# Kernel tuning notes

Measured on AMD Instinct MI355X. Metric: run time of the kernel, lower is better.

Reference implementation:

```python
import jax, jax.numpy as jnp
import numpy as np

H, I, E, TOPK = 2048, 4096, 8, 2
B, S = 2, 2048

def setup_inputs() -> dict:
    key = jax.random.key(0)
    ks = jax.random.split(key, 6)
    x = jax.random.normal(ks[0], (B, S, H), dtype=jnp.float32)
    expert_indices = jax.random.randint(ks[1], (B, S, TOPK), 0, E, dtype=jnp.int64)
    expert_weights = jax.random.uniform(ks[2], (B, S, TOPK), dtype=jnp.float32)
    gate_proj = jax.random.normal(ks[3], (E, I, H), dtype=jnp.float32) * 0.02
    up_proj = jax.random.normal(ks[4], (E, I, H), dtype=jnp.float32) * 0.02
    down_proj = jax.random.normal(ks[5], (E, H, I), dtype=jnp.float32) * 0.02
    return {"x": x, "expert_indices": expert_indices, "expert_weights": expert_weights,
            "gate_proj": gate_proj, "up_proj": up_proj, "down_proj": down_proj}

def reference(x, expert_indices, expert_weights, gate_proj, up_proj, down_proj):
    b, s, h = x.shape
    T = b * s
    xf = x.reshape(T, h)                                   # [T, H]
    idx = expert_indices.reshape(T, -1)                    # [T, K]
    w = expert_weights.reshape(T, -1)                      # [T, K]
    n_exp = gate_proj.shape[0]
    # Per-token combined weight for each expert (sums duplicate slots, matching
    # the original weighted scatter-add over (token, slot) pairs).
    onehot = jax.nn.one_hot(idx, n_exp, dtype=xf.dtype)    # [T, K, E]
    we = jnp.einsum('tk,tke->et', w, onehot)               # [E, T]

    def step(acc, inp):
        g_w, u_w, d_w, w_e = inp                           # [I,H], [I,H], [H,I], [T]
        g = xf @ g_w.T                                     # [T, I]
        u = xf @ u_w.T                                     # [T, I]
        inter = g * jax.nn.sigmoid(g) * u                  # fused SiLU(g) * u
        acc = acc + w_e[:, None] * (inter @ d_w.T)         # weighted combine
        return acc, None

    out0 = jnp.zeros((T, h), dtype=x.dtype)
    out, _ = jax.lax.scan(step, out0, (gate_proj, up_proj, down_proj, we))
    return out.reshape(b, s, h)
```

## Files before the change

### kernel.cpp

```cpp
#include <hip/hip_runtime.h>
#include <hip/hip_bf16.h>
#include <stdint.h>

#define H_DIM 2048
#define I_DIM 4096
#define NEXP  8
#define NTOK  4096
#define NPAIR 8192
#define PAD_ROWS (NPAIR + 256)

#define MiB (1024ull * 1024ull)
#define WS_COUNTS   0ull
#define WS_OFFSETS  256ull
#define WS_TOKID    1024ull
#define WS_SLOT     (64ull * 1024)
#define WS_PAIRW    (128ull * 1024)
#define WS_XG       (1ull * MiB)
#define WS_INTER    (36ull * MiB)
#define WS_Y        (104ull * MiB)
#define WS_GW       (176ull * MiB)
#define WS_UW       (304ull * MiB)
#define WS_DW       (432ull * MiB)
#define WS_FULL     (560ull * MiB)

typedef __attribute__((ext_vector_type(8))) short bf16x8;
typedef __attribute__((ext_vector_type(4))) float f32x4;

#if defined(__has_builtin)
#if __has_builtin(__builtin_amdgcn_cvt_pk_bf16_f32)
#define HAVE_CVT_PK 1
#endif
#endif

__device__ __forceinline__ uint32_t bf16_bits_rne(float x) {
  uint32_t u = __float_as_uint(x);
  return (u + 0x7FFFu + ((u >> 16) & 1u)) >> 16;
}
__device__ __forceinline__ uint32_t pk_bf16(float a, float b) {
#ifdef HAVE_CVT_PK
  auto r = __builtin_amdgcn_cvt_pk_bf16_f32(a, b);
  return __builtin_bit_cast(uint32_t, r);
#else
  return bf16_bits_rne(a) | (bf16_bits_rne(b) << 16);
#endif
}
__device__ __forceinline__ uint16_t bf16_one(float x) {
  return (uint16_t)(pk_bf16(x, x) & 0xFFFFu);
}

__device__ __forceinline__ void async_load16(const void* g, void* l) {
  __builtin_amdgcn_global_load_lds(
      (const __attribute__((address_space(1))) void*)g,
      (__attribute__((address_space(3))) void*)l, 16, 0, 0);
}

#define WAIT_VM6()   do { asm volatile("s_waitcnt vmcnt(6)" ::: "memory"); __builtin_amdgcn_sched_barrier(0); } while (0)
#define WAIT_VM0()   do { asm volatile("s_waitcnt vmcnt(0)" ::: "memory"); __builtin_amdgcn_sched_barrier(0); } while (0)
#define WAIT_LGKM0() do { asm volatile("s_waitcnt lgkmcnt(0)" ::: "memory"); __builtin_amdgcn_sched_barrier(0); } while (0)
#define BARRIER()    do { __builtin_amdgcn_s_barrier(); asm volatile("" ::: "memory"); } while (0)

__global__ void route_kernel(const int* __restrict__ idx, const float* __restrict__ wts,
                             int* __restrict__ ws_counts, int* __restrict__ ws_offsets,
                             int* __restrict__ tokid, int* __restrict__ slotOf,
                             float* __restrict__ pairw) {
  __shared__ int s_cnt[NEXP], s_off[NEXP], s_cur[NEXP];
  int tid = threadIdx.x;
  if (tid < NEXP) s_cnt[tid] = 0;
  __syncthreads();
  for (int p = tid; p < NPAIR; p += 256) atomicAdd(&s_cnt[idx[p]], 1);
  __syncthreads();
  if (tid == 0) {
    int acc = 0;
    for (int e = 0; e < NEXP; e++) { s_off[e] = acc; s_cur[e] = acc; acc += s_cnt[e]; }
  }
  __syncthreads();
  for (int p = tid; p < NPAIR; p += 256) {
    int e = idx[p];
    int slot = atomicAdd(&s_cur[e], 1);
    tokid[slot] = p >> 1;
    slotOf[p] = slot;
    pairw[slot] = wts[p];
  }
  if (tid < NEXP) { ws_counts[tid] = s_cnt[tid]; ws_offsets[tid] = s_off[tid]; }
}

__global__ void gather_cast_kernel(const float* __restrict__ x, const int* __restrict__ tokid,
                                   uint16_t* __restrict__ xg) {
  int p = blockIdx.x;
  int t = tokid[p];
  int c = threadIdx.x * 8;
  const float4* src = (const float4*)(x + (size_t)t * H_DIM + c);
  float4 v0 = src[0], v1 = src[1];
  uint4 o;
  o.x = pk_bf16(v0.x, v0.y); o.y = pk_bf16(v0.z, v0.w);
  o.z = pk_bf16(v1.x, v1.y); o.w = pk_bf16(v1.z, v1.w);
  *(uint4*)(xg + (size_t)p * H_DIM + c) = o;
}

__global__ void cast3_kernel(const float* __restrict__ g, const float* __restrict__ u,
                             const float* __restrict__ d,
                             uint16_t* __restrict__ gw, uint16_t* __restrict__ uw,
                             uint16_t* __restrict__ dw) {
  const float* src = blockIdx.y == 0 ? g : (blockIdx.y == 1 ? u : d);
  uint16_t*    dst = blockIdx.y == 0 ? gw : (blockIdx.y == 1 ? uw : dw);
  const long long n8 = (long long)NEXP * I_DIM * H_DIM / 8;
  long long stride = (long long)gridDim.x * blockDim.x;
  for (long long i = (long long)blockIdx.x * blockDim.x + threadIdx.x; i < n8; i += stride) {
    const float4* s = (const float4*)(src + i * 8);
    float4 a = s[0], b = s[1];
    uint4 o = { pk_bf16(a.x, a.y), pk_bf16(a.z, a.w), pk_bf16(b.x, b.y), pk_bf16(b.z, b.w) };
    *(uint4*)(dst + i * 8) = o;
  }
}

#define T1_A    (256 * 64)
#define T1_B    (64 * 64)
#define T1_ELE  (T1_A + 2 * T1_B)

__global__ __launch_bounds__(512, 1)
void gemm1_v5(const uint16_t* __restrict__ xg,
              const uint16_t* __restrict__ gw, const uint16_t* __restrict__ uw,
              const int* __restrict__ ws_counts, const int* __restrict__ ws_offsets,
              uint16_t* __restrict__ inter) {
  int e = blockIdx.z;
  int cnt = ws_counts[e];
  int rowTile = blockIdx.y;
  if (rowTile * 256 >= cnt) return;
  int off = ws_offsets[e];
  int colBase = blockIdx.x * 64;
  size_t rowBase = (size_t)off + (size_t)rowTile * 256;

  __shared__ uint16_t lds[3 * T1_ELE];

  int tid = threadIdx.x, lane = tid & 63, w = tid >> 6;
  int r8 = lane >> 3;
  int gsw = ((lane & 7) ^ r8) << 3;

  const uint16_t* srcA[4];
#pragma unroll
  for (int c = 0; c < 4; c++)
    srcA[c] = xg + (rowBase + (size_t)(w * 32 + c * 8 + r8)) * H_DIM + gsw;
  const uint16_t* srcG = gw + ((size_t)e * I_DIM + colBase + w * 8 + r8) * H_DIM + gsw;
  const uint16_t* srcU = uw + ((size_t)e * I_DIM + colBase + w * 8 + r8) * H_DIM + gsw;

  const int dA = w * 2048;
  const int dG = T1_A + w * 512;
  const int dU = T1_A + T1_B + w * 512;

  f32x4 accg[4][2], accu[4][2];
  f32x4 zero = {0.f, 0.f, 0.f, 0.f};
#pragma unroll
  for (int mi = 0; mi < 4; mi++)
#pragma unroll
    for (int ni = 0; ni < 2; ni++) { accg[mi][ni] = zero; accu[mi][ni] = zero; }

  int wr = w >> 1, wc = w & 1;
  int wm = wr * 64, wn = wc * 32;
  int lcol = lane & 15, quad = lane >> 4;
  int sx = (lcol & 7) << 3;

  auto STG = [&](int kt, int b) {
    uint16_t* lb = lds + b * T1_ELE;
    int ko = kt * 64;
#pragma unroll
    for (int c = 0; c < 4; c++) async_load16(srcA[c] + ko, lb + dA + c * 512);
    async_load16(srcG + ko, lb + dG);
    async_load16(srcU + ko, lb + dU);
  };

  STG(0, 0); STG(1, 1);
  WAIT_VM6();
  BARRIER();

  const int NT = H_DIM / 64;
  for (int t = 0; t < NT; ++t) {
    const int b = t % 3, b2 = (t + 2) % 3;
    uint16_t* lb  = lds + b * T1_ELE;
    uint16_t* lb2 = lds + b2 * T1_ELE;
    const bool pre = (t + 2 < NT);
    const int ko = (t + 2) * 64;

    {
      const int krs = (quad * 8) ^ sx;
      bf16x8 af[4], bg_[2], bu_[2];
#pragma unroll
      for (int mi = 0; mi < 4; mi++)
        af[mi] = *(const bf16x8*)(lb + (wm + mi * 16 + lcol) * 64 + krs);
#pragma unroll
      for (int ni = 0; ni < 2; ni++) {
        bg_[ni] = *(const bf16x8*)(lb + T1_A + (wn + ni * 16 + lcol) * 64 + krs);
        bu_[ni] = *(const bf16x8*)(lb + T1_A + T1_B + (wn + ni * 16 + lcol) * 64 + krs);
      }
      if (pre) {
        async_load16(srcA[0] + ko, lb2 + dA + 0 * 512);
        async_load16(srcA[1] + ko, lb2 + dA + 1 * 512);
        async_load16(srcA[2] + ko, lb2 + dA + 2 * 512);
      }
      BARRIER();
      WAIT_LGKM0();
      __builtin_amdgcn_s_setprio(1);
#pragma unroll
      for (int mi = 0; mi < 4; mi++)
#pragma unroll
        for (int ni = 0; ni < 2; ni++) {
          accg[mi][ni] = __builtin_amdgcn_mfma_f32_16x16x32_bf16(af[mi], bg_[ni], accg[mi][ni], 0, 0, 0);
          accu[mi][ni] = __builtin_amdgcn_mfma_f32_16x16x32_bf16(af[mi], bu_[ni], accu[mi][ni], 0, 0, 0);
        }
      __builtin_amdgcn_s_setprio(0);
      BARRIER();
    }
    {
      const int krs = (32 + quad * 8) ^ sx;
      bf16x8 af[4], bg_[2], bu_[2];
#pragma unroll
      for (int mi = 0; mi < 4; mi++)
        af[mi] = *(const bf16x8*)(lb + (wm + mi * 16 + lcol) * 64 + krs);
#pragma unroll
      for (int ni = 0; ni < 2; ni++) {
        bg_[ni] = *(const bf16x8*)(lb + T1_A + (wn + ni * 16 + lcol) * 64 + krs);
        bu_[ni] = *(const bf16x8*)(lb + T1_A + T1_B + (wn + ni * 16 + lcol) * 64 + krs);
      }
      if (pre) {
        async_load16(srcA[3] + ko, lb2 + dA + 3 * 512);
        async_load16(srcG + ko, lb2 + dG);
        async_load16(srcU + ko, lb2 + dU);
      }
      BARRIER();
      WAIT_LGKM0();
      __builtin_amdgcn_s_setprio(1);
#pragma unroll
      for (int mi = 0; mi < 4; mi++)
#pragma unroll
        for (int ni = 0; ni < 2; ni++) {
          accg[mi][ni] = __builtin_amdgcn_mfma_f32_16x16x32_bf16(af[mi], bg_[ni], accg[mi][ni], 0, 0, 0);
          accu[mi][ni] = __builtin_amdgcn_mfma_f32_16x16x32_bf16(af[mi], bu_[ni], accu[mi][ni], 0, 0, 0);
        }
      __builtin_amdgcn_s_setprio(0);
      if (pre) { WAIT_VM6(); } else { WAIT_VM0(); }
      BARRIER();
    }
  }

  int col0 = colBase + wn;
#pragma unroll
  for (int mi = 0; mi < 4; mi++) {
#pragma unroll
    for (int r = 0; r < 4; r++) {
      int localRow = rowTile * 256 + wm + mi * 16 + quad * 4 + r;
      if (localRow < cnt) {
        size_t prow = (size_t)off + localRow;
#pragma unroll
        for (int ni = 0; ni < 2; ni++) {
          float g = accg[mi][ni][r], u = accu[mi][ni][r];
          float v = (g / (1.f + __expf(-g))) * u;
          inter[prow * I_DIM + col0 + ni * 16 + lcol] = bf16_one(v);
        }
      }
    }
  }
}

#define T2_A    (256 * 64)
#define T2_B    (128 * 64)
#define T2_ELE  (T2_A + T2_B)

__global__ __launch_bounds__(512, 1)
void gemm2_v5(const uint16_t* __restrict__ inter, const uint16_t* __restrict__ dw,
              const int* __restrict__ ws_counts, const int* __restrict__ ws_offsets,
              const float* __restrict__ pairw, float* __restrict__ y) {
  int e = blockIdx.z;
  int cnt = ws_counts[e];
  int rowTile = blockIdx.y;
  if (rowTile * 256 >= cnt) return;
  int off = ws_offsets[e];
  int colBase = blockIdx.x * 128;
  size_t rowBase = (size_t)off + (size_t)rowTile * 256;

  __shared__ uint16_t lds[3 * T2_ELE];

  int tid = threadIdx.x, lane = tid & 63, w = tid >> 6;
  int r8 = lane >> 3;
  int gsw = ((lane & 7) ^ r8) << 3;

  const uint16_t* srcA[4];
#pragma unroll
  for (int c = 0; c < 4; c++)
    srcA[c] = inter + (rowBase + (size_t)(w * 32 + c * 8 + r8)) * I_DIM + gsw;
  const uint16_t* srcB[2];
#pragma unroll
  for (int c = 0; c < 2; c++)
    srcB[c] = dw + ((size_t)e * H_DIM + colBase + w * 16 + c * 8 + r8) * I_DIM + gsw;

  const int dA = w * 2048;
  const int dB = T2_A + w * 1024;

  f32x4 acc[4][4];
  f32x4 zero = {0.f, 0.f, 0.f, 0.f};
#pragma unroll
  for (int mi = 0; mi < 4; mi++)
#pragma unroll
    for (int ni = 0; ni < 4; ni++) acc[mi][ni] = zero;

  int wr = w >> 1, wc = w & 1;
  int wm = wr * 64, wn = wc * 64;
  int lcol = lane & 15, quad = lane >> 4;
  int sx = (lcol & 7) << 3;

  auto STG = [&](int kt, int b) {
    uint16_t* lb = lds + b * T2_ELE;
    int ko = kt * 64;
#pragma unroll
    for (int c = 0; c < 4; c++) async_load16(srcA[c] + ko, lb + dA + c * 512);
#pragma unroll
    for (int c = 0; c < 2; c++) async_load16(srcB[c] + ko, lb + dB + c * 512);
  };

  STG(0, 0); STG(1, 1);
  WAIT_VM6();
  BARRIER();

  const int NT = I_DIM / 64;
  for (int t = 0; t < NT; ++t) {
    const int b = t % 3, b2 = (t + 2) % 3;
    uint16_t* lb  = lds + b * T2_ELE;
    uint16_t* lb2 = lds + b2 * T2_ELE;
    const bool pre = (t + 2 < NT);
    const int ko = (t + 2) * 64;

    {
      const int krs = (quad * 8) ^ sx;
      bf16x8 af[4], bb[4];
#pragma unroll
      for (int mi = 0; mi < 4; mi++)
        af[mi] = *(const bf16x8*)(lb + (wm + mi * 16 + lcol) * 64 + krs);
#pragma unroll
      for (int ni = 0; ni < 4; ni++)
        bb[ni] = *(const bf16x8*)(lb + T2_A + (wn + ni * 16 + lcol) * 64 + krs);
      if (pre) {
        async_load16(srcA[0] + ko, lb2 + dA + 0 * 512);
        async_load16(srcA[1] + ko, lb2 + dA + 1 * 512);
        async_load16(srcA[2] + ko, lb2 + dA + 2 * 512);
      }
      BARRIER();
      WAIT_LGKM0();
      __builtin_amdgcn_s_setprio(1);
#pragma unroll
      for (int mi = 0; mi < 4; mi++)
#pragma unroll
        for (int ni = 0; ni < 4; ni++)
          acc[mi][ni] = __builtin_amdgcn_mfma_f32_16x16x32_bf16(af[mi], bb[ni], acc[mi][ni], 0, 0, 0);
      __builtin_amdgcn_s_setprio(0);
      BARRIER();
    }
    {
      const int krs = (32 + quad * 8) ^ sx;
      bf16x8 af[4], bb[4];
#pragma unroll
      for (int mi = 0; mi < 4; mi++)
        af[mi] = *(const bf16x8*)(lb + (wm + mi * 16 + lcol) * 64 + krs);
#pragma unroll
      for (int ni = 0; ni < 4; ni++)
        bb[ni] = *(const bf16x8*)(lb + T2_A + (wn + ni * 16 + lcol) * 64 + krs);
      if (pre) {
        async_load16(srcA[3] + ko, lb2 + dA + 3 * 512);
        async_load16(srcB[0] + ko, lb2 + dB + 0 * 512);
        async_load16(srcB[1] + ko, lb2 + dB + 1 * 512);
      }
      BARRIER();
      WAIT_LGKM0();
      __builtin_amdgcn_s_setprio(1);
#pragma unroll
      for (int mi = 0; mi < 4; mi++)
#pragma unroll
        for (int ni = 0; ni < 4; ni++)
          acc[mi][ni] = __builtin_amdgcn_mfma_f32_16x16x32_bf16(af[mi], bb[ni], acc[mi][ni], 0, 0, 0);
      __builtin_amdgcn_s_setprio(0);
      if (pre) { WAIT_VM6(); } else { WAIT_VM0(); }
      BARRIER();
    }
  }

  int col0 = colBase + wn;
#pragma unroll
  for (int mi = 0; mi < 4; mi++) {
#pragma unroll
    for (int r = 0; r < 4; r++) {
      int localRow = rowTile * 256 + wm + mi * 16 + quad * 4 + r;
      if (localRow < cnt) {
        size_t prow = (size_t)off + localRow;
        float wgt = pairw[prow];
        float* yr = y + prow * H_DIM + col0;
#pragma unroll
        for (int ni = 0; ni < 4; ni++)
          yr[ni * 16 + lcol] = acc[mi][ni][r] * wgt;
      }
    }
  }
}

__global__ void combine_kernel(const float* __restrict__ y, const int* __restrict__ slotOf,
                               float* __restrict__ out) {
  int t = blockIdx.x;
  int s0 = slotOf[2 * t], s1 = slotOf[2 * t + 1];
  int c = threadIdx.x * 8;
  const float4* a = (const float4*)(y + (size_t)s0 * H_DIM + c);
  const float4* b = (const float4*)(y + (size_t)s1 * H_DIM + c);
  float4 a0 = a[0], a1 = a[1], b0 = b[0], b1 = b[1];
  float4 o0 = {a0.x + b0.x, a0.y + b0.y, a0.z + b0.z, a0.w + b0.w};
  float4 o1 = {a1.x + b1.x, a1.y + b1.y, a1.z + b1.z, a1.w + b1.w};
  float4* dst = (float4*)(out + (size_t)t * H_DIM + c);
  dst[0] = o0; dst[1] = o1;
}

extern "C" void kernel_launch(void* const* d_in, const int* in_sizes, int n_in,
                              void* d_out, int out_size, void* d_ws, size_t ws_size,
                              hipStream_t stream) {
  const float* x    = (const float*)d_in[0];
  const int*   eidx = (const int*)d_in[1];
  const float* ew   = (const float*)d_in[2];
  const float* gate = (const float*)d_in[3];
  const float* up   = (const float*)d_in[4];
  const float* down = (const float*)d_in[5];
  float* out = (float*)d_out;
  char* ws = (char*)d_ws;

  if (ws_size < WS_FULL) {
    hipMemsetAsync(d_out, 0, (size_t)NTOK * H_DIM * sizeof(float), stream);
    return;
  }

  int*      counts  = (int*)(ws + WS_COUNTS);
  int*      offsets = (int*)(ws + WS_OFFSETS);
  int*      tokid   = (int*)(ws + WS_TOKID);
  int*      slotOf  = (int*)(ws + WS_SLOT);
  float*    pairw   = (float*)(ws + WS_PAIRW);
  uint16_t* xg      = (uint16_t*)(ws + WS_XG);
  uint16_t* inter   = (uint16_t*)(ws + WS_INTER);
  float*    y       = (float*)(ws + WS_Y);
  uint16_t* gw      = (uint16_t*)(ws + WS_GW);
  uint16_t* uw      = (uint16_t*)(ws + WS_UW);
  uint16_t* dwp     = (uint16_t*)(ws + WS_DW);

  route_kernel<<<1, 256, 0, stream>>>(eidx, ew, counts, offsets, tokid, slotOf, pairw);
  gather_cast_kernel<<<NPAIR, 256, 0, stream>>>(x, tokid, xg);
  cast3_kernel<<<dim3(2048, 3), 256, 0, stream>>>(gate, up, down, gw, uw, dwp);

  gemm1_v5<<<dim3(I_DIM / 64, NPAIR / 256, NEXP), 512, 0, stream>>>(
      xg, gw, uw, counts, offsets, inter);
  gemm2_v5<<<dim3(H_DIM / 128, NPAIR / 256, NEXP), 512, 0, stream>>>(
      inter, dwp, counts, offsets, pairw, y);
  combine_kernel<<<NTOK, 256, 0, stream>>>(y, slotOf, out);
}
```

Measured before the change: 1.312 ms.

## Remap GEMM block IDs across XCDs and simplify gemm1 pipeline to one barrier

Both GEMMs now launch a 1D grid and remap the linear block index so that consecutive blocks, which are dispatched round-robin across the 8 XCDs, land on the same expert and row tile within one XCD. The aim is better L2 reuse of the expert weights and activations. gemm1 also replaces its split half-step prefetch, which had three barriers per K tile, with a single prefetch of tile t+2 at the start of each iteration and one barrier at the end. This cuts synchronisation, but the loads and MFMAs may interleave less finely.

Measured after the change: 1.381 ms. +5.2%, slower.

```diff
diff --git a/kernel.cpp b/kernel.cpp
--- a/kernel.cpp
+++ b/kernel.cpp
@@ -118,17 +118,21 @@
 #define T1_ELE  (T1_A + 2 * T1_B)
 
 __global__ __launch_bounds__(512, 1)
-void gemm1_v5(const uint16_t* __restrict__ xg,
+void gemm1_v6(const uint16_t* __restrict__ xg,
               const uint16_t* __restrict__ gw, const uint16_t* __restrict__ uw,
               const int* __restrict__ ws_counts, const int* __restrict__ ws_offsets,
               uint16_t* __restrict__ inter) {
-  int e = blockIdx.z;
+  int lin = blockIdx.x;
+  int wid = (lin & 7) * 2048 + (lin >> 3);
+  int bx = wid & 63;
+  int by = (wid >> 6) & 31;
+  int e  = wid >> 11;
+
   int cnt = ws_counts[e];
-  int rowTile = blockIdx.y;
-  if (rowTile * 256 >= cnt) return;
+  if (by * 256 >= cnt) return;
   int off = ws_offsets[e];
-  int colBase = blockIdx.x * 64;
-  size_t rowBase = (size_t)off + (size_t)rowTile * 256;
+  int colBase = bx * 64;
+  size_t rowBase = (size_t)off + (size_t)by * 256;
 
   __shared__ uint16_t lds[3 * T1_ELE];
 
@@ -154,34 +158,31 @@
 #pragma unroll
     for (int ni = 0; ni < 2; ni++) { accg[mi][ni] = zero; accu[mi][ni] = zero; }
 
+  auto STG = [&](int kt, int b) {
+    uint16_t* lb = lds + b * T1_ELE;
+    int ko = kt * 64;
+#pragma unroll
+    for (int c = 0; c < 4; c++) async_load16(srcA[c] + ko, lb + dA + c * 512);
+    async_load16(srcG + ko, lb + dG);
+    async_load16(srcU + ko, lb + dU);
+  };
+
+  STG(0, 0); STG(1, 1);
+  WAIT_VM6();
+  BARRIER();
+
   int wr = w >> 1, wc = w & 1;
   int wm = wr * 64, wn = wc * 32;
   int lcol = lane & 15, quad = lane >> 4;
   int sx = (lcol & 7) << 3;
 
-  auto STG = [&](int kt, int b) {
-    uint16_t* lb = lds + b * T1_ELE;
-    int ko = kt * 64;
-#pragma unroll
-    for (int c = 0; c < 4; c++) async_load16(srcA[c] + ko, lb + dA + c * 512);
-    async_load16(srcG + ko, lb + dG);
-    async_load16(srcU + ko, lb + dU);
-  };
-
-  STG(0, 0); STG(1, 1);
-  WAIT_VM6();
-  BARRIER();
-
   const int NT = H_DIM / 64;
   for (int t = 0; t < NT; ++t) {
-    const int b = t % 3, b2 = (t + 2) % 3;
-    uint16_t* lb  = lds + b * T1_ELE;
-    uint16_t* lb2 = lds + b2 * T1_ELE;
-    const bool pre = (t + 2 < NT);
-    const int ko = (t + 2) * 64;
-
-    {
-      const int krs = (quad * 8) ^ sx;
+    if (t + 2 < NT) STG(t + 2, (t + 2) % 3);
+    const uint16_t* lb = lds + (t % 3) * T1_ELE;
+#pragma unroll
+    for (int ks = 0; ks < 2; ks++) {
+      int krs = (ks * 32 + quad * 8) ^ sx;
       bf16x8 af[4], bg_[2], bu_[2];
 #pragma unroll
       for (int mi = 0; mi < 4; mi++)
@@ -191,13 +192,6 @@
         bg_[ni] = *(const bf16x8*)(lb + T1_A + (wn + ni * 16 + lcol) * 64 + krs);
         bu_[ni] = *(const bf16x8*)(lb + T1_A + T1_B + (wn + ni * 16 + lcol) * 64 + krs);
       }
-      if (pre) {
-        async_load16(srcA[0] + ko, lb2 + dA + 0 * 512);
-        async_load16(srcA[1] + ko, lb2 + dA + 1 * 512);
-        async_load16(srcA[2] + ko, lb2 + dA + 2 * 512);
-      }
-      BARRIER();
-      WAIT_LGKM0();
       __builtin_amdgcn_s_setprio(1);
 #pragma unroll
       for (int mi = 0; mi < 4; mi++)
@@ -207,38 +201,9 @@
           accu[mi][ni] = __builtin_amdgcn_mfma_f32_16x16x32_bf16(af[mi], bu_[ni], accu[mi][ni], 0, 0, 0);
         }
       __builtin_amdgcn_s_setprio(0);
-      BARRIER();
     }
-    {
-      const int krs = (32 + quad * 8) ^ sx;
-      bf16x8 af[4], bg_[2], bu_[2];
-#pragma unroll
-      for (int mi = 0; mi < 4; mi++)
-        af[mi] = *(const bf16x8*)(lb + (wm + mi * 16 + lcol) * 64 + krs);
-#pragma unroll
-      for (int ni = 0; ni < 2; ni++) {
-        bg_[ni] = *(const bf16x8*)(lb + T1_A + (wn + ni * 16 + lcol) * 64 + krs);
-        bu_[ni] = *(const bf16x8*)(lb + T1_A + T1_B + (wn + ni * 16 + lcol) * 64 + krs);
-      }
-      if (pre) {
-        async_load16(srcA[3] + ko, lb2 + dA + 3 * 512);
-        async_load16(srcG + ko, lb2 + dG);
-        async_load16(srcU + ko, lb2 + dU);
-      }
-      BARRIER();
-      WAIT_LGKM0();
-      __builtin_amdgcn_s_setprio(1);
-#pragma unroll
-      for (int mi = 0; mi < 4; mi++)
-#pragma unroll
-        for (int ni = 0; ni < 2; ni++) {
-          accg[mi][ni] = __builtin_amdgcn_mfma_f32_16x16x32_bf16(af[mi], bg_[ni], accg[mi][ni], 0, 0, 0);
-          accu[mi][ni] = __builtin_amdgcn_mfma_f32_16x16x32_bf16(af[mi], bu_[ni], accu[mi][ni], 0, 0, 0);
-        }
-      __builtin_amdgcn_s_setprio(0);
-      if (pre) { WAIT_VM6(); } else { WAIT_VM0(); }
-      BARRIER();
-    }
+    if (t + 2 < NT) { WAIT_VM6(); } else { WAIT_VM0(); }
+    BARRIER();
   }
 
   int col0 = colBase + wn;
@@ -246,7 +211,7 @@
   for (int mi = 0; mi < 4; mi++) {
 #pragma unroll
     for (int r = 0; r < 4; r++) {
-      int localRow = rowTile * 256 + wm + mi * 16 + quad * 4 + r;
+      int localRow = by * 256 + wm + mi * 16 + quad * 4 + r;
       if (localRow < cnt) {
         size_t prow = (size_t)off + localRow;
 #pragma unroll
@@ -265,16 +230,20 @@
 #define T2_ELE  (T2_A + T2_B)
 
 __global__ __launch_bounds__(512, 1)
-void gemm2_v5(const uint16_t* __restrict__ inter, const uint16_t* __restrict__ dw,
+void gemm2_v6(const uint16_t* __restrict__ inter, const uint16_t* __restrict__ dw,
               const int* __restrict__ ws_counts, const int* __restrict__ ws_offsets,
               const float* __restrict__ pairw, float* __restrict__ y) {
-  int e = blockIdx.z;
+  int lin = blockIdx.x;
+  int wid = (lin & 7) * 512 + (lin >> 3);
+  int bx = wid & 15;
+  int by = (wid >> 4) & 31;
+  int e  = wid >> 9;
+
   int cnt = ws_counts[e];
-  int rowTile = blockIdx.y;
-  if (rowTile * 256 >= cnt) return;
+  if (by * 256 >= cnt) return;
   int off = ws_offsets[e];
-  int colBase = blockIdx.x * 128;
-  size_t rowBase = (size_t)off + (size_t)rowTile * 256;
+  int colBase = bx * 128;
+  size_t rowBase = (size_t)off + (size_t)by * 256;
 
   __shared__ uint16_t lds[3 * T2_ELE];
 
@@ -385,7 +354,7 @@
   for (int mi = 0; mi < 4; mi++) {
 #pragma unroll
     for (int r = 0; r < 4; r++) {
-      int localRow = rowTile * 256 + wm + mi * 16 + quad * 4 + r;
+      int localRow = by * 256 + wm + mi * 16 + quad * 4 + r;
       if (localRow < cnt) {
         size_t prow = (size_t)off + localRow;
         float wgt = pairw[prow];
@@ -445,9 +414,9 @@
   gather_cast_kernel<<<NPAIR, 256, 0, stream>>>(x, tokid, xg);
   cast3_kernel<<<dim3(2048, 3), 256, 0, stream>>>(gate, up, down, gw, uw, dwp);
 
-  gemm1_v5<<<dim3(I_DIM / 64, NPAIR / 256, NEXP), 512, 0, stream>>>(
+  gemm1_v6<<<dim3(64 * 32 * NEXP), 512, 0, stream>>>(
       xg, gw, uw, counts, offsets, inter);
-  gemm2_v5<<<dim3(H_DIM / 128, NPAIR / 256, NEXP), 512, 0, stream>>>(
+  gemm2_v6<<<dim3(16 * 32 * NEXP), 512, 0, stream>>>(
       inter, dwp, counts, offsets, pairw, y);
   combine_kernel<<<NTOK, 256, 0, stream>>>(y, slotOf, out);
 }
```
